# Kernel tuning notes

Measured on AMD Instinct MI355X. Metric: run time of the kernel, lower is better.

Reference implementation:

```python
import jax, jax.numpy as jnp
import numpy as np

QMAX = 127.0  # int8 symmetric
EPS = 1e-8


def _fake_quant(v, scale):
    # quantize/clamp/dequantize with straight-through rounding (STE clip)
    s = jnp.maximum(scale, EPS)
    scaled = v / s
    clipped = jnp.clip(scaled, -QMAX, QMAX)
    q = clipped + jax.lax.stop_gradient(jnp.round(clipped) - clipped)
    return q * s


def setup_inputs() -> dict:
    key = jax.random.key(0)
    kx, kw, kb = jax.random.split(key, 3)
    B, S, D_IN, D_OUT = 8, 2048, 4096, 4096
    x = jax.random.normal(kx, (B, S, D_IN), dtype=jnp.float32)
    weight = jax.random.normal(kw, (D_OUT, D_IN), dtype=jnp.float32) * 0.02
    bias = jax.random.normal(kb, (D_OUT,), dtype=jnp.float32) * 0.02
    return {"x": x, "weight": weight, "bias": bias}


def reference(x, weight, bias):
    # activation: dynamic per-tensor symmetric int8 fake-quant
    a_scale = jnp.max(jnp.abs(x)) / QMAX
    xq = _fake_quant(x, a_scale)
    # weight: per-channel (output-channel axis 0) symmetric int8 fake-quant
    w_scale = jnp.max(jnp.abs(weight), axis=1, keepdims=True) / QMAX  # [out, 1]
    wq = _fake_quant(weight, w_scale)
    # F.linear: y = x @ W^T + b
    return jnp.einsum('bsd,od->bso', xq, wq) + bias
```

## Files before the change

### kernel.cpp

```cpp
#include <hip/hip_runtime.h>
#include <hip/hip_bf16.h>
#include <stdint.h>


#define QMAX_F 127.0f
#define EPS_F 1e-8f

typedef int v4i __attribute__((ext_vector_type(4)));

static constexpr size_t WSCALE_OFF = 64;
static constexpr size_t XQ_OFF = 1u << 16;

__device__ __forceinline__ int quant1m(float v, float rs) {
    float t = v * rs;
    t = fminf(fmaxf(t, -QMAX_F), QMAX_F);
    return (int)rintf(t);
}

__global__ void prep_kernel(const float4* __restrict__ x, int nx4,
                            const float4* __restrict__ w, int* __restrict__ wq,
                            float* __restrict__ w_scale, int K4,
                            unsigned* __restrict__ amax) {
    const int t = threadIdx.x;
    const int row = blockIdx.x;

    float xm = 0.0f;
    for (int i = blockIdx.x * 256 + t; i < nx4; i += gridDim.x * 256) {
        float4 v = x[i];
        xm = fmaxf(xm, fmaxf(fmaxf(fabsf(v.x), fabsf(v.y)), fmaxf(fabsf(v.z), fabsf(v.w))));
    }

    const float4* wr = w + (size_t)row * K4;
    float4 vals[4];
    float wm = 0.0f;
    for (int i = 0; i < 4; i++) {
        float4 v = wr[t + 256 * i];
        vals[i] = v;
        wm = fmaxf(wm, fmaxf(fmaxf(fabsf(v.x), fabsf(v.y)), fmaxf(fabsf(v.z), fabsf(v.w))));
    }

    for (int off = 32; off > 0; off >>= 1) {
        xm = fmaxf(xm, __shfl_xor(xm, off));
        wm = fmaxf(wm, __shfl_xor(wm, off));
    }
    __shared__ float sx[4], sw[4];
    if ((t & 63) == 0) { sx[t >> 6] = xm; sw[t >> 6] = wm; }
    __syncthreads();
    float xb = fmaxf(fmaxf(sx[0], sx[1]), fmaxf(sx[2], sx[3]));
    float wb = fmaxf(fmaxf(sw[0], sw[1]), fmaxf(sw[2], sw[3]));
    if (t == 0) atomicMax(amax, __float_as_uint(xb));

    float s = fmaxf(wb / QMAX_F, EPS_F);
    if (t == 0) w_scale[row] = s;
    float rs = 1.0f / s;
    int* wqr = wq + (size_t)row * K4;
    for (int i = 0; i < 4; i++) {
        float4 v = vals[i];
        int q0 = quant1m(v.x, rs), q1 = quant1m(v.y, rs), q2 = quant1m(v.z, rs), q3 = quant1m(v.w, rs);
        wqr[t + 256 * i] = (q0 & 0xff) | ((q1 & 0xff) << 8) | ((q2 & 0xff) << 16) | ((q3 & 0xff) << 24);
    }
}

__global__ void quantx_kernel(const float4* __restrict__ x, const unsigned* __restrict__ amax,
                              int* __restrict__ xq, int n4) {
    float s = fmaxf(__uint_as_float(*amax) / QMAX_F, EPS_F);
    float rs = 1.0f / s;
    int tid = blockIdx.x * blockDim.x + threadIdx.x;
    int stride = gridDim.x * blockDim.x;
    for (int i = n4 - 1 - tid; i >= 0; i -= stride) {
        float4 v = x[i];
        int q0 = quant1m(v.x, rs), q1 = quant1m(v.y, rs), q2 = quant1m(v.z, rs), q3 = quant1m(v.w, rs);
        xq[i] = (q0 & 0xff) | ((q1 & 0xff) << 8) | ((q2 & 0xff) << 16) | ((q3 & 0xff) << 24);
    }
}

#define BM 256
#define BN 256
#define BKB 128

__device__ __forceinline__ void gload16(const char* g, char* l) {
    __builtin_amdgcn_global_load_lds(
        (const __attribute__((address_space(1))) void*)g,
        (__attribute__((address_space(3))) void*)l, 16, 0, 0);
}

__global__ __launch_bounds__(512, 2) void gemm_i8_8ph(
    const char* __restrict__ xq, const char* __restrict__ wq,
    const float* __restrict__ w_scale, const unsigned* __restrict__ amax,
    const float* __restrict__ bias, float* __restrict__ out,
    int M, int N, int K) {
    __shared__ __align__(16) char lds[131072];

    const int nwg = gridDim.x, bid = blockIdx.x;
    const int cpx = nwg >> 3;
    const int swz = (bid & 7) * cpx + (bid >> 3);
    const int nbm = M / BM;
    const int bm = swz % nbm, bn = swz / nbm;

    const int t = threadIdx.x;
    const int lane = t & 63, wid = t >> 6;
    const int wr = wid >> 2, wc = wid & 3;

    const int srow = t >> 3;
    const int scol = ((t & 7) ^ (srow & 7)) << 4;
    const char* aSrc = xq + (size_t)(bm * BM + srow) * K + scol;
    const char* bSrc = wq + (size_t)(bn * BN + srow) * K + scol;
    char* ldsT = lds + t * 16;

    auto stageA = [&](int half, int tt, int ktc) {
        char* d = ldsT + ((unsigned)(tt & 1) << 16) + ((unsigned)half << 14);
        gload16(aSrc + (size_t)(half * 128) * K + ktc, d);
        gload16(aSrc + (size_t)(half * 128 + 64) * K + ktc, d + 8192);
    };
    auto stageB = [&](int half, int tt, int ktc) {
        char* d = ldsT + ((unsigned)(tt & 1) << 16) + 32768u + ((unsigned)half << 14);
        gload16(bSrc + (size_t)(half * 128) * K + ktc, d);
        gload16(bSrc + (size_t)(half * 128 + 64) * K + ktc, d + 8192);
    };

    const int rA = lane & 15, kg = lane >> 4, sw7 = lane & 7;
    const unsigned cks0 = (unsigned)((kg ^ sw7) << 4);
    const unsigned cks1 = (unsigned)(((4 + kg) ^ sw7) << 4);
    const unsigned aBase = ((unsigned)wr << 14) + ((unsigned)rA << 7);
    const unsigned bBase = 32768u + ((unsigned)wc << 13) + ((unsigned)rA << 7);

    v4i acc[8][4];
#pragma unroll
    for (int m = 0; m < 8; m++)
#pragma unroll
        for (int n = 0; n < 4; n++) acc[m][n] = (v4i){0, 0, 0, 0};

    const int nkt = K / BKB;

    stageA(0, 0, 0); stageA(1, 0, 0); stageB(0, 0, 0); stageB(1, 0, 0);
    {
        const int k1 = (1 < nkt) ? BKB : 0;
        stageB(0, 1, k1); stageA(0, 1, k1); stageB(1, 1, k1);
    }
    asm volatile("s_waitcnt vmcnt(6)" ::: "memory");
    __builtin_amdgcn_s_barrier();

    for (int T = 0; T < nkt; ++T) {
        const unsigned bb = (unsigned)(T & 1) << 16;
        const int kA1 = (T + 1 < nkt) ? (T + 1) * BKB : 0;
        const int kT2 = (T + 2 < nkt) ? (T + 2) * BKB : 0;
        v4i a[4][2], b0[2][2], b1[2][2];

#pragma unroll
        for (int m = 0; m < 4; m++) {
            a[m][0] = *(const v4i*)(lds + bb + aBase + ((unsigned)m << 11) + cks0);
            a[m][1] = *(const v4i*)(lds + bb + aBase + ((unsigned)m << 11) + cks1);
        }
#pragma unroll
        for (int n = 0; n < 2; n++) {
            b0[n][0] = *(const v4i*)(lds + bb + bBase + ((unsigned)n << 11) + cks0);
            b0[n][1] = *(const v4i*)(lds + bb + bBase + ((unsigned)n << 11) + cks1);
        }
        stageA(1, T + 1, kA1);
        __builtin_amdgcn_s_barrier();
        asm volatile("s_waitcnt lgkmcnt(0)" ::: "memory");
        __builtin_amdgcn_sched_barrier(0);
        __builtin_amdgcn_s_setprio(1);
#pragma unroll
        for (int ks = 0; ks < 2; ks++)
#pragma unroll
            for (int m = 0; m < 4; m++)
#pragma unroll
                for (int n = 0; n < 2; n++)
                    acc[m][n] = __builtin_amdgcn_mfma_i32_16x16x64_i8(a[m][ks], b0[n][ks], acc[m][n], 0, 0, 0);
        __builtin_amdgcn_s_setprio(0);

#pragma unroll
        for (int n = 0; n < 2; n++) {
            b1[n][0] = *(const v4i*)(lds + bb + bBase + 4096u + ((unsigned)n << 11) + cks0);
            b1[n][1] = *(const v4i*)(lds + bb + bBase + 4096u + ((unsigned)n << 11) + cks1);
        }
        __builtin_amdgcn_s_barrier();
        asm volatile("s_waitcnt lgkmcnt(0)" ::: "memory");
        __builtin_amdgcn_sched_barrier(0);
        __builtin_amdgcn_s_setprio(1);
#pragma unroll
        for (int ks = 0; ks < 2; ks++)
#pragma unroll
            for (int m = 0; m < 4; m++)
#pragma unroll
                for (int n = 0; n < 2; n++)
                    acc[m][2 + n] = __builtin_amdgcn_mfma_i32_16x16x64_i8(a[m][ks], b1[n][ks], acc[m][2 + n], 0, 0, 0);
        __builtin_amdgcn_s_setprio(0);

#pragma unroll
        for (int m = 0; m < 4; m++) {
            a[m][0] = *(const v4i*)(lds + bb + aBase + 8192u + ((unsigned)m << 11) + cks0);
            a[m][1] = *(const v4i*)(lds + bb + aBase + 8192u + ((unsigned)m << 11) + cks1);
        }
        __builtin_amdgcn_s_barrier();
        asm volatile("s_waitcnt lgkmcnt(0)" ::: "memory");
        __builtin_amdgcn_sched_barrier(0);
        __builtin_amdgcn_s_setprio(1);
#pragma unroll
        for (int ks = 0; ks < 2; ks++)
#pragma unroll
            for (int m = 0; m < 4; m++)
#pragma unroll
                for (int n = 0; n < 2; n++)
                    acc[4 + m][2 + n] = __builtin_amdgcn_mfma_i32_16x16x64_i8(a[m][ks], b1[n][ks], acc[4 + m][2 + n], 0, 0, 0);
        __builtin_amdgcn_s_setprio(0);

        stageB(0, T + 2, kT2);
        stageA(0, T + 2, kT2);
        stageB(1, T + 2, kT2);
        asm volatile("s_waitcnt vmcnt(6)" ::: "memory");
        __builtin_amdgcn_s_barrier();
        __builtin_amdgcn_s_setprio(1);
#pragma unroll
        for (int ks = 0; ks < 2; ks++)
#pragma unroll
            for (int m = 0; m < 4; m++)
#pragma unroll
                for (int n = 0; n < 2; n++)
                    acc[4 + m][n] = __builtin_amdgcn_mfma_i32_16x16x64_i8(a[m][ks], b0[n][ks], acc[4 + m][n], 0, 0, 0);
        __builtin_amdgcn_s_setprio(0);
    }

    float a_s = fmaxf(__uint_as_float(*amax) / QMAX_F, EPS_F);
    const int row0 = bm * BM + wr * 128;
    const int col0 = bn * BN + wc * 64;
#pragma unroll
    for (int n = 0; n < 4; n++) {
        int col = col0 + n * 16 + rA;
        float f = a_s * w_scale[col];
        float bv = bias[col];
#pragma unroll
        for (int m = 0; m < 8; m++) {
            int row = row0 + m * 16 + (kg << 2);
            size_t base = (size_t)row * N + col;
#pragma unroll
            for (int j = 0; j < 4; j++)
                out[base + (size_t)j * N] = (float)acc[m][n][j] * f + bv;
        }
    }
}

extern "C" void kernel_launch(void* const* d_in, const int* in_sizes, int n_in,
                              void* d_out, int out_size, void* d_ws, size_t ws_size,
                              hipStream_t stream) {
    const float* x = (const float*)d_in[0];
    const float* w = (const float*)d_in[1];
    const float* bias = (const float*)d_in[2];
    float* out = (float*)d_out;

    const int N = in_sizes[2];
    const int K = in_sizes[1] / N;
    const int M = in_sizes[0] / K;

    char* ws = (char*)d_ws;
    unsigned* amax = (unsigned*)ws;
    float* w_scale = (float*)(ws + WSCALE_OFF);
    char* xq = ws + XQ_OFF;
    char* wq = ws + XQ_OFF + (size_t)M * K;

    size_t needed = XQ_OFF + (size_t)M * K + (size_t)N * K;
    if (ws_size < needed) return;

    hipMemsetAsync(amax, 0, 4, stream);

    int n4x = (M * K) / 4;
    prep_kernel<<<N, 256, 0, stream>>>((const float4*)x, n4x, (const float4*)w,
                                       (int*)wq, w_scale, K / 4, amax);
    quantx_kernel<<<2048, 256, 0, stream>>>((const float4*)x, amax, (int*)xq, n4x);

    int grid = (M / BM) * (N / BN);
    gemm_i8_8ph<<<grid, 512, 0, stream>>>(xq, wq, w_scale, amax, bias, out, M, N, K);
}
```

Measured before the change: 428.7 us.

## Switch int8 GEMM inner loop from 16x16x64 to 32x32x32 MFMA tiles

Replaces the 16x16x64 int8 MFMA instructions with 32x32x32 variants, reorganizing per-wave accumulators into 4x2 tiles of 32x32 and reworking LDS fragment addressing and the epilogue row mapping. Larger MFMA tiles mean fewer instructions and fewer LDS fragment reads per unit of work, which should raise arithmetic intensity per LDS load. The risk is different LDS bank conflict behaviour from the new swizzled address pattern, and a less coalesced epilogue store layout.

```diff
diff --git a/kernel.cpp b/kernel.cpp
--- a/kernel.cpp
+++ b/kernel.cpp
@@ -7,6 +7,7 @@
 #define EPS_F 1e-8f
 
 typedef int v4i __attribute__((ext_vector_type(4)));
+typedef int v16i __attribute__((ext_vector_type(16)));
 
 static constexpr size_t WSCALE_OFF = 64;
 static constexpr size_t XQ_OFF = 1u << 16;
@@ -84,7 +85,7 @@
         (__attribute__((address_space(3))) void*)l, 16, 0, 0);
 }
 
-__global__ __launch_bounds__(512, 2) void gemm_i8_8ph(
+__global__ __launch_bounds__(512, 2) void gemm_i8_32(
     const char* __restrict__ xq, const char* __restrict__ wq,
     const float* __restrict__ w_scale, const unsigned* __restrict__ amax,
     const float* __restrict__ bias, float* __restrict__ out,
@@ -118,17 +119,20 @@
         gload16(bSrc + (size_t)(half * 128 + 64) * K + ktc, d + 8192);
     };
 
-    const int rA = lane & 15, kg = lane >> 4, sw7 = lane & 7;
-    const unsigned cks0 = (unsigned)((kg ^ sw7) << 4);
-    const unsigned cks1 = (unsigned)(((4 + kg) ^ sw7) << 4);
-    const unsigned aBase = ((unsigned)wr << 14) + ((unsigned)rA << 7);
-    const unsigned bBase = 32768u + ((unsigned)wc << 13) + ((unsigned)rA << 7);
-
-    v4i acc[8][4];
-#pragma unroll
-    for (int m = 0; m < 8; m++)
-#pragma unroll
-        for (int n = 0; n < 4; n++) acc[m][n] = (v4i){0, 0, 0, 0};
+    const int r32 = lane & 31, kh = lane >> 5, sw7 = r32 & 7;
+    unsigned cks[4];
+#pragma unroll
+    for (int ks = 0; ks < 4; ks++) cks[ks] = (unsigned)(((2 * ks + kh) ^ sw7) << 4);
+    const unsigned aB = ((unsigned)wr << 14) + ((unsigned)r32 << 7);
+    const unsigned bB = 32768u + ((unsigned)wc << 13) + ((unsigned)r32 << 7);
+
+    v16i acc[4][2];
+#pragma unroll
+    for (int mi = 0; mi < 4; mi++)
+#pragma unroll
+        for (int ni = 0; ni < 2; ni++)
+#pragma unroll
+            for (int r = 0; r < 16; r++) acc[mi][ni][r] = 0;
 
     const int nkt = K / BKB;
 
@@ -144,66 +148,56 @@
         const unsigned bb = (unsigned)(T & 1) << 16;
         const int kA1 = (T + 1 < nkt) ? (T + 1) * BKB : 0;
         const int kT2 = (T + 2 < nkt) ? (T + 2) * BKB : 0;
-        v4i a[4][2], b0[2][2], b1[2][2];
-
-#pragma unroll
-        for (int m = 0; m < 4; m++) {
-            a[m][0] = *(const v4i*)(lds + bb + aBase + ((unsigned)m << 11) + cks0);
-            a[m][1] = *(const v4i*)(lds + bb + aBase + ((unsigned)m << 11) + cks1);
-        }
-#pragma unroll
-        for (int n = 0; n < 2; n++) {
-            b0[n][0] = *(const v4i*)(lds + bb + bBase + ((unsigned)n << 11) + cks0);
-            b0[n][1] = *(const v4i*)(lds + bb + bBase + ((unsigned)n << 11) + cks1);
-        }
+        v4i a[2][4], b0[4], b1[4];
+
+#pragma unroll
+        for (int mi = 0; mi < 2; mi++)
+#pragma unroll
+            for (int ks = 0; ks < 4; ks++)
+                a[mi][ks] = *(const v4i*)(lds + bb + aB + ((unsigned)mi << 12) + cks[ks]);
+#pragma unroll
+        for (int ks = 0; ks < 4; ks++)
+            b0[ks] = *(const v4i*)(lds + bb + bB + cks[ks]);
         stageA(1, T + 1, kA1);
         __builtin_amdgcn_s_barrier();
         asm volatile("s_waitcnt lgkmcnt(0)" ::: "memory");
         __builtin_amdgcn_sched_barrier(0);
         __builtin_amdgcn_s_setprio(1);
 #pragma unroll
-        for (int ks = 0; ks < 2; ks++)
-#pragma unroll
-            for (int m = 0; m < 4; m++)
-#pragma unroll
-                for (int n = 0; n < 2; n++)
-                    acc[m][n] = __builtin_amdgcn_mfma_i32_16x16x64_i8(a[m][ks], b0[n][ks], acc[m][n], 0, 0, 0);
-        __builtin_amdgcn_s_setprio(0);
-
-#pragma unroll
-        for (int n = 0; n < 2; n++) {
-            b1[n][0] = *(const v4i*)(lds + bb + bBase + 4096u + ((unsigned)n << 11) + cks0);
-            b1[n][1] = *(const v4i*)(lds + bb + bBase + 4096u + ((unsigned)n << 11) + cks1);
-        }
+        for (int ks = 0; ks < 4; ks++)
+#pragma unroll
+            for (int mi = 0; mi < 2; mi++)
+                acc[mi][0] = __builtin_amdgcn_mfma_i32_32x32x32_i8(a[mi][ks], b0[ks], acc[mi][0], 0, 0, 0);
+        __builtin_amdgcn_s_setprio(0);
+
+#pragma unroll
+        for (int ks = 0; ks < 4; ks++)
+            b1[ks] = *(const v4i*)(lds + bb + bB + 4096u + cks[ks]);
         __builtin_amdgcn_s_barrier();
         asm volatile("s_waitcnt lgkmcnt(0)" ::: "memory");
         __builtin_amdgcn_sched_barrier(0);
         __builtin_amdgcn_s_setprio(1);
 #pragma unroll
-        for (int ks = 0; ks < 2; ks++)
-#pragma unroll
-            for (int m = 0; m < 4; m++)
-#pragma unroll
-                for (int n = 0; n < 2; n++)
-                    acc[m][2 + n] = __builtin_amdgcn_mfma_i32_16x16x64_i8(a[m][ks], b1[n][ks], acc[m][2 + n], 0, 0, 0);
-        __builtin_amdgcn_s_setprio(0);
-
-#pragma unroll
-        for (int m = 0; m < 4; m++) {
-            a[m][0] = *(const v4i*)(lds + bb + aBase + 8192u + ((unsigned)m << 11) + cks0);
-            a[m][1] = *(const v4i*)(lds + bb + aBase + 8192u + ((unsigned)m << 11) + cks1);
-        }
+        for (int ks = 0; ks < 4; ks++)
+#pragma unroll
+            for (int mi = 0; mi < 2; mi++)
+                acc[mi][1] = __builtin_amdgcn_mfma_i32_32x32x32_i8(a[mi][ks], b1[ks], acc[mi][1], 0, 0, 0);
+        __builtin_amdgcn_s_setprio(0);
+
+#pragma unroll
+        for (int mi = 0; mi < 2; mi++)
+#pragma unroll
+            for (int ks = 0; ks < 4; ks++)
+                a[mi][ks] = *(const v4i*)(lds + bb + aB + 8192u + ((unsigned)mi << 12) + cks[ks]);
         __builtin_amdgcn_s_barrier();
         asm volatile("s_waitcnt lgkmcnt(0)" ::: "memory");
         __builtin_amdgcn_sched_barrier(0);
         __builtin_amdgcn_s_setprio(1);
 #pragma unroll
-        for (int ks = 0; ks < 2; ks++)
-#pragma unroll
-            for (int m = 0; m < 4; m++)
-#pragma unroll
-                for (int n = 0; n < 2; n++)
-                    acc[4 + m][2 + n] = __builtin_amdgcn_mfma_i32_16x16x64_i8(a[m][ks], b1[n][ks], acc[4 + m][2 + n], 0, 0, 0);
+        for (int ks = 0; ks < 4; ks++)
+#pragma unroll
+            for (int mi = 0; mi < 2; mi++)
+                acc[2 + mi][1] = __builtin_amdgcn_mfma_i32_32x32x32_i8(a[mi][ks], b1[ks], acc[2 + mi][1], 0, 0, 0);
         __builtin_amdgcn_s_setprio(0);
 
         stageB(0, T + 2, kT2);
@@ -213,30 +207,28 @@
         __builtin_amdgcn_s_barrier();
         __builtin_amdgcn_s_setprio(1);
 #pragma unroll
-        for (int ks = 0; ks < 2; ks++)
-#pragma unroll
-            for (int m = 0; m < 4; m++)
-#pragma unroll
-                for (int n = 0; n < 2; n++)
-                    acc[4 + m][n] = __builtin_amdgcn_mfma_i32_16x16x64_i8(a[m][ks], b0[n][ks], acc[4 + m][n], 0, 0, 0);
+        for (int ks = 0; ks < 4; ks++)
+#pragma unroll
+            for (int mi = 0; mi < 2; mi++)
+                acc[2 + mi][0] = __builtin_amdgcn_mfma_i32_32x32x32_i8(a[mi][ks], b0[ks], acc[2 + mi][0], 0, 0, 0);
         __builtin_amdgcn_s_setprio(0);
     }
 
     float a_s = fmaxf(__uint_as_float(*amax) / QMAX_F, EPS_F);
     const int row0 = bm * BM + wr * 128;
-    const int col0 = bn * BN + wc * 64;
-#pragma unroll
-    for (int n = 0; n < 4; n++) {
-        int col = col0 + n * 16 + rA;
+    const int col0 = bn * BN + wc * 64 + r32;
+#pragma unroll
+    for (int ni = 0; ni < 2; ni++) {
+        int col = col0 + ni * 32;
         float f = a_s * w_scale[col];
         float bv = bias[col];
 #pragma unroll
-        for (int m = 0; m < 8; m++) {
-            int row = row0 + m * 16 + (kg << 2);
-            size_t base = (size_t)row * N + col;
-#pragma unroll
-            for (int j = 0; j < 4; j++)
-                out[base + (size_t)j * N] = (float)acc[m][n][j] * f + bv;
+        for (int mi = 0; mi < 4; mi++) {
+#pragma unroll
+            for (int r = 0; r < 16; r++) {
+                int row = row0 + mi * 32 + (r & 3) + 8 * (r >> 2) + 4 * kh;
+                out[(size_t)row * N + col] = (float)acc[mi][ni][r] * f + bv;
+            }
         }
     }
 }
@@ -270,5 +262,5 @@
     quantx_kernel<<<2048, 256, 0, stream>>>((const float4*)x, amax, (int*)xq, n4x);
 
     int grid = (M / BM) * (N / BN);
-    gemm_i8_8ph<<<grid, 512, 0, stream>>>(xq, wq, w_scale, amax, bias, out, M, N, K);
-}
+    gemm_i8_32<<<grid, 512, 0, stream>>>(xq, wq, w_scale, amax, bias, out, M, N, K);
+}
```

After: 447.1 us. 4.3% more time.
